# Kernel tuning notes

Hardware: AMD Instinct MI355X
Metric: run time of the kernel (lower is better)

Reference implementation:

```python
import jax, jax.numpy as jnp
import numpy as np

B, T, D, H = 2, 2048, 2048, 16


def setup_inputs() -> dict:
    key = jax.random.key(0)
    ks = jax.random.split(key, 5)
    s = 0.02  # typical init scale
    return {
        "x": jax.random.normal(ks[0], (B, T, D), jnp.float32),
        "wq": jax.random.normal(ks[1], (D, D), jnp.float32) * s,
        "wk": jax.random.normal(ks[2], (D, D), jnp.float32) * s,
        "wv": jax.random.normal(ks[3], (D, D), jnp.float32) * s,
        "wo": jax.random.normal(ks[4], (D, D), jnp.float32) * s,
    }


def weight_quant(w):
    # BitNet ternary-ish quant: sign(w) * mean(|w|), straight-through estimator
    scale = jnp.maximum(jnp.mean(jnp.abs(w)), 1e-5)
    q = jnp.sign(w) * scale
    return jax.lax.stop_gradient(q) + w - jax.lax.stop_gradient(w)


def reference(x, wq, wk, wv, wo):
    b, t, c = x.shape
    h = H
    hd = c // h
    # F.linear: y = x @ w.T  (weight shape [out, in])
    def proj(w):
        y = jnp.einsum('btc,dc->btd', x, weight_quant(w))
        return y.reshape(b, t, h, hd).transpose(0, 2, 1, 3)  # [b,h,t,hd]

    q, k, v = proj(wq), proj(wk), proj(wv)
    scale = 1.0 / np.sqrt(hd).astype(np.float32)
    scores = jnp.einsum('bhqd,bhkd->bhqk', q, k) * scale
    causal = jnp.tril(jnp.ones((t, t), dtype=bool))
    scores = jnp.where(causal, scores, jnp.finfo(scores.dtype).min)
    att = jax.nn.softmax(scores, axis=-1)
    y = jnp.einsum('bhqk,bhkd->bhqd', att, v)
    y = y.transpose(0, 2, 1, 3).reshape(b, t, c)
    return jnp.einsum('btc,dc->btd', y, weight_quant(wo))
```

## Files before the change

### kernel.cpp

```cpp
#include <hip/hip_runtime.h>
#include <stdint.h>

#define D_MODEL 2048
#define SEQ     2048
#define BATCH   2
#define NH      16
#define HD      128
#define M_TOT   (BATCH*SEQ)
#define NELEM_W (D_MODEL*D_MODEL)

typedef float f32x4 __attribute__((ext_vector_type(4)));
typedef short bf16x8 __attribute__((ext_vector_type(8)));

__device__ __forceinline__ unsigned short f2bf(float f) {
  union { float f; uint32_t u; } v; v.f = f;
  uint32_t r = v.u + 0x7FFFu + ((v.u >> 16) & 1u);
  return (unsigned short)(r >> 16);
}

__device__ __forceinline__ void gload_lds16(const unsigned short* g, unsigned short* l) {
  __builtin_amdgcn_global_load_lds(
      (const __attribute__((address_space(1))) unsigned int*)g,
      (__attribute__((address_space(3))) unsigned int*)l, 16, 0, 0);
}

__global__ __launch_bounds__(256) void reduce1(const float* w0, const float* w1,
                                               const float* w2, const float* w3,
                                               float* partials) {
  const int wi = blockIdx.y;
  const float* w = (wi == 0) ? w0 : (wi == 1) ? w1 : (wi == 2) ? w2 : w3;
  const float4* w4 = (const float4*)w;
  const int t = threadIdx.x, bx = blockIdx.x;
  float s = 0.f;
  #pragma unroll
  for (int i = 0; i < 16; ++i) {
    float4 v = w4[(size_t)bx * 4096 + i * 256 + t];
    s += fabsf(v.x) + fabsf(v.y) + fabsf(v.z) + fabsf(v.w);
  }
  #pragma unroll
  for (int off = 32; off; off >>= 1) s += __shfl_down(s, off);
  __shared__ float sm[4];
  if ((t & 63) == 0) sm[t >> 6] = s;
  __syncthreads();
  if (t == 0) partials[wi * 256 + bx] = sm[0] + sm[1] + sm[2] + sm[3];
}

__global__ __launch_bounds__(256) void reduce2(const float* partials, float* scales) {
  const int wi = blockIdx.x, t = threadIdx.x;
  float s = partials[wi * 256 + t];
  #pragma unroll
  for (int off = 32; off; off >>= 1) s += __shfl_down(s, off);
  __shared__ float sm[4];
  if ((t & 63) == 0) sm[t >> 6] = s;
  __syncthreads();
  if (t == 0) scales[wi] = fmaxf((sm[0] + sm[1] + sm[2] + sm[3]) * (1.f / 4194304.f), 1e-5f);
}

__global__ __launch_bounds__(256) void cvt_x(const float* x, unsigned short* xb) {
  const int i = blockIdx.x * 256 + threadIdx.x;
  float4 v = ((const float4*)x)[i];
  ushort4 o;
  o.x = f2bf(v.x); o.y = f2bf(v.y); o.z = f2bf(v.z); o.w = f2bf(v.w);
  ((ushort4*)xb)[i] = o;
}

__global__ __launch_bounds__(256) void sign_w(const float* w0, const float* w1,
                                              const float* w2, const float* w3,
                                              unsigned short* signs) {
  const int wi = blockIdx.y;
  const float* w = (wi == 0) ? w0 : (wi == 1) ? w1 : (wi == 2) ? w2 : w3;
  unsigned short* o = signs + (size_t)wi * NELEM_W;
  const int i = blockIdx.x * 256 + threadIdx.x;
  float4 v = ((const float4*)w)[i];
  ushort4 s;
  s.x = (v.x > 0.f) ? 0x3F80u : ((v.x < 0.f) ? 0xBF80u : 0u);
  s.y = (v.y > 0.f) ? 0x3F80u : ((v.y < 0.f) ? 0xBF80u : 0u);
  s.z = (v.z > 0.f) ? 0x3F80u : ((v.z < 0.f) ? 0xBF80u : 0u);
  s.w = (v.w > 0.f) ? 0x3F80u : ((v.w < 0.f) ? 0xBF80u : 0u);
  ((ushort4*)o)[i] = s;
}

template <int MODE>
__global__ __launch_bounds__(256) void gemm_bt(const unsigned short* __restrict__ A,
                                               const unsigned short* __restrict__ W,
                                               void* __restrict__ outp,
                                               const float* __restrict__ scales,
                                               int sidx, float extra) {
  constexpr int K = 2048;
  __shared__ alignas(16) unsigned short ldsA[128 * 64];
  __shared__ alignas(16) unsigned short ldsB[128 * 64];
  const int t = threadIdx.x;
  const int wid = t >> 6, lane = t & 63;
  const int llo = lane & 15, lhi = lane >> 4;
  const int m0 = blockIdx.y * 128, n0 = blockIdx.x * 128;
  const int wm = (wid >> 1) * 64, wn = (wid & 1) * 64;
  f32x4 acc[4][4] = {};

  for (int kt = 0; kt < K / 64; ++kt) {
    const int k0 = kt * 64;
    #pragma unroll
    for (int i = 0; i < 4; ++i) {
      const int idx = i * 256 + t;
      const int row = idx >> 3, slot = idx & 7;
      const int ksw = k0 + ((slot ^ (row & 7)) << 3);
      gload_lds16(A + (size_t)(m0 + row) * K + ksw, &ldsA[(i * 256 + wid * 64) * 8]);
      gload_lds16(W + (size_t)(n0 + row) * K + ksw, &ldsB[(i * 256 + wid * 64) * 8]);
    }
    __syncthreads();
    #pragma unroll
    for (int kk = 0; kk < 2; ++kk) {
      bf16x8 a[4], b[4];
      #pragma unroll
      for (int f = 0; f < 4; ++f) {
        const int ra = wm + f * 16 + llo;
        a[f] = *(const bf16x8*)&ldsA[ra * 64 + ((kk * 4 + lhi) ^ (ra & 7)) * 8];
        const int rb = wn + f * 16 + llo;
        b[f] = *(const bf16x8*)&ldsB[rb * 64 + ((kk * 4 + lhi) ^ (rb & 7)) * 8];
      }
      #pragma unroll
      for (int fm = 0; fm < 4; ++fm)
        #pragma unroll
        for (int fn = 0; fn < 4; ++fn)
          acc[fm][fn] = __builtin_amdgcn_mfma_f32_16x16x32_bf16(a[fm], b[fn], acc[fm][fn], 0, 0, 0);
    }
    __syncthreads();
  }

  const float sc = scales[sidx] * extra;
  #pragma unroll
  for (int fm = 0; fm < 4; ++fm)
    #pragma unroll
    for (int fn = 0; fn < 4; ++fn)
      #pragma unroll
      for (int r = 0; r < 4; ++r) {
        const int row = m0 + wm + fm * 16 + lhi * 4 + r;
        const int col = n0 + wn + fn * 16 + llo;
        const float v = acc[fm][fn][r] * sc;
        if (MODE == 2) {
          ((float*)outp)[(size_t)row * D_MODEL + col] = v;
        } else {
          const int b = row >> 11, tt = row & 2047, h = col >> 7, d = col & 127;
          size_t idx;
          if (MODE == 0) idx = ((size_t)((b * NH + h) * SEQ + tt)) * HD + d;
          else           idx = ((size_t)((b * NH + h) * HD + d)) * SEQ + tt;
          ((unsigned short*)outp)[idx] = f2bf(v);
        }
      }
}

__global__ __launch_bounds__(512, 4) void attn_fwd(const unsigned short* __restrict__ Q,
                                                   const unsigned short* __restrict__ Kt,
                                                   const unsigned short* __restrict__ VT,
                                                   unsigned short* __restrict__ O) {
  __shared__ alignas(16) unsigned short lds[2][16384];
  __shared__ alignas(16) unsigned short plds[8][1024];
  const int t = threadIdx.x;
  const int wid = t >> 6, lane = t & 63;
  const int llo = lane & 15, lhi = lane >> 4;
  const int bh = blockIdx.x;
  const int g = 15 - (int)blockIdx.y;
  const int qbase = g * 128;
  const int nt = 2 * g + 2;
  const size_t bh_td = (size_t)bh * SEQ * HD;
  const size_t bh_dt = (size_t)bh * HD * SEQ;
  unsigned short* pw = &plds[wid][0];
  const int fvl = (llo & 7) ^ ((llo & 8) >> 1);

  auto stage = [&](int buf, int j) {
    const int t0 = j * 64;
    #pragma unroll
    for (int i = 0; i < 2; ++i) {
      const int c = i * 512 + t;
      const int row = c >> 4, slot = c & 15;
      gload_lds16(Kt + bh_td + (size_t)(t0 + row) * HD + ((slot ^ (row & 15)) << 3),
                  &lds[buf][(size_t)(i * 512 + wid * 64) * 8]);
    }
    #pragma unroll
    for (int i = 0; i < 2; ++i) {
      const int c = i * 512 + t;
      const int vrow = c >> 3, vslot = c & 7;
      const int fv = (vrow & 7) ^ ((vrow & 8) >> 1);
      gload_lds16(VT + bh_dt + (size_t)vrow * SEQ + t0 + ((vslot ^ fv) << 3),
                  &lds[buf][8192 + (size_t)(i * 512 + wid * 64) * 8]);
    }
  };

  bf16x8 qa[4];
  {
    const unsigned short* qp = Q + bh_td + (size_t)(qbase + wid * 16 + llo) * HD + lhi * 8;
    #pragma unroll
    for (int kk = 0; kk < 4; ++kk) qa[kk] = *(const bf16x8*)(qp + kk * 32);
  }
  f32x4 oacc[8] = {};
  float m_r[4], l_r[4];
  #pragma unroll
  for (int r = 0; r < 4; ++r) { m_r[r] = -1e30f; l_r[r] = 0.f; }

  stage(0, 0);
  for (int j = 0; j < nt; ++j) {
    const int cur = j & 1;
    __syncthreads();
    if (j + 1 < nt) stage(cur ^ 1, j + 1);
    f32x4 s[4] = {};
    __builtin_amdgcn_s_setprio(1);
    #pragma unroll
    for (int nb = 0; nb < 4; ++nb) {
      const int row = nb * 16 + llo;
      #pragma unroll
      for (int kk = 0; kk < 4; ++kk) {
        const bf16x8 kb = *(const bf16x8*)&lds[cur][row * 128 + (((kk * 4 + lhi) ^ llo) << 3)];
        s[nb] = __builtin_amdgcn_mfma_f32_16x16x32_bf16(qa[kk], kb, s[nb], 0, 0, 0);
      }
    }
    __builtin_amdgcn_s_setprio(0);
    if (j >= nt - 2) {
      #pragma unroll
      for (int nb = 0; nb < 4; ++nb)
        #pragma unroll
        for (int r = 0; r < 4; ++r)
          if (j * 64 + nb * 16 + llo > qbase + wid * 16 + lhi * 4 + r) s[nb][r] = -1e30f;
    }
    float mx[4], al[4], ps[4];
    #pragma unroll
    for (int r = 0; r < 4; ++r)
      mx[r] = fmaxf(fmaxf(s[0][r], s[1][r]), fmaxf(s[2][r], s[3][r]));
    #pragma unroll
    for (int off = 1; off < 16; off <<= 1)
      #pragma unroll
      for (int r = 0; r < 4; ++r) mx[r] = fmaxf(mx[r], __shfl_xor(mx[r], off));
    #pragma unroll
    for (int r = 0; r < 4; ++r) {
      const float mn = fmaxf(m_r[r], mx[r]);
      al[r] = __expf(m_r[r] - mn);
      m_r[r] = mn;
      #pragma unroll
      for (int nb = 0; nb < 4; ++nb) s[nb][r] = __expf(s[nb][r] - mn);
      ps[r] = (s[0][r] + s[1][r]) + (s[2][r] + s[3][r]);
    }
    #pragma unroll
    for (int off = 1; off < 16; off <<= 1)
      #pragma unroll
      for (int r = 0; r < 4; ++r) ps[r] += __shfl_xor(ps[r], off);
    #pragma unroll
    for (int r = 0; r < 4; ++r) l_r[r] = l_r[r] * al[r] + ps[r];
    #pragma unroll
    for (int nb = 0; nb < 8; ++nb)
      #pragma unroll
      for (int r = 0; r < 4; ++r) oacc[nb][r] *= al[r];
    #pragma unroll
    for (int nb = 0; nb < 4; ++nb)
      #pragma unroll
      for (int r = 0; r < 4; ++r) {
        const int q = lhi * 4 + r;
        const int slot = nb * 2 + (llo >> 3);
        pw[q * 64 + ((slot ^ (q & 7)) << 3) + (llo & 7)] = f2bf(s[nb][r]);
      }
    asm volatile("s_waitcnt lgkmcnt(0)" ::: "memory");
    __builtin_amdgcn_sched_barrier(0);
    const bf16x8 pa0 = *(const bf16x8*)&pw[llo * 64 + ((lhi ^ (llo & 7)) << 3)];
    const bf16x8 pa1 = *(const bf16x8*)&pw[llo * 64 + (((4 + lhi) ^ (llo & 7)) << 3)];
    __builtin_amdgcn_s_setprio(1);
    #pragma unroll
    for (int db = 0; db < 8; ++db) {
      const unsigned short* vbp = &lds[cur][8192 + (db * 16 + llo) * 64];
      const bf16x8 vb0 = *(const bf16x8*)&vbp[(lhi ^ fvl) << 3];
      const bf16x8 vb1 = *(const bf16x8*)&vbp[((4 + lhi) ^ fvl) << 3];
      oacc[db] = __builtin_amdgcn_mfma_f32_16x16x32_bf16(pa0, vb0, oacc[db], 0, 0, 0);
      oacc[db] = __builtin_amdgcn_mfma_f32_16x16x32_bf16(pa1, vb1, oacc[db], 0, 0, 0);
    }
    __builtin_amdgcn_s_setprio(0);
  }

  const int b = bh >> 4, h = bh & 15;
  float inv[4];
  #pragma unroll
  for (int r = 0; r < 4; ++r) inv[r] = 1.f / l_r[r];
  #pragma unroll
  for (int db = 0; db < 8; ++db)
    #pragma unroll
    for (int r = 0; r < 4; ++r) {
      const int qi = qbase + wid * 16 + lhi * 4 + r;
      const int d = db * 16 + llo;
      O[((size_t)(b * SEQ + qi)) * D_MODEL + h * HD + d] = f2bf(oacc[db][r] * inv[r]);
    }
}

extern "C" void kernel_launch(void* const* d_in, const int* in_sizes, int n_in,
                              void* d_out, int out_size, void* d_ws, size_t ws_size,
                              hipStream_t stream) {
  const float* x  = (const float*)d_in[0];
  const float* wq = (const float*)d_in[1];
  const float* wk = (const float*)d_in[2];
  const float* wv = (const float*)d_in[3];
  const float* wo = (const float*)d_in[4];

  char* ws = (char*)d_ws;
  float* scales   = (float*)ws;
  float* partials = (float*)(ws + 256);
  unsigned short* xbf   = (unsigned short*)(ws + 8192);
  const size_t nMD = (size_t)M_TOT * D_MODEL;
  unsigned short* signs = xbf + nMD;
  unsigned short* Qb = signs + 4 * (size_t)NELEM_W;
  unsigned short* Kb = Qb + nMD;
  unsigned short* Vt = Kb + nMD;
  unsigned short* Ab = Vt + nMD;

  reduce1<<<dim3(256, 4), 256, 0, stream>>>(wq, wk, wv, wo, partials);
  reduce2<<<dim3(4), 256, 0, stream>>>(partials, scales);
  cvt_x<<<dim3(8192), 256, 0, stream>>>(x, xbf);
  sign_w<<<dim3(4096, 4), 256, 0, stream>>>(wq, wk, wv, wo, signs);

  gemm_bt<0><<<dim3(16, 32), 256, 0, stream>>>(xbf, signs,                       (void*)Qb, scales, 0, 0.08838834764831845f);
  gemm_bt<0><<<dim3(16, 32), 256, 0, stream>>>(xbf, signs + (size_t)NELEM_W,     (void*)Kb, scales, 1, 1.0f);
  gemm_bt<1><<<dim3(16, 32), 256, 0, stream>>>(xbf, signs + 2 * (size_t)NELEM_W, (void*)Vt, scales, 2, 1.0f);

  attn_fwd<<<dim3(32, 16), 512, 0, stream>>>(Qb, Kb, Vt, Ab);

  gemm_bt<2><<<dim3(16, 32), 256, 0, stream>>>(Ab, signs + 3 * (size_t)NELEM_W, d_out, scales, 3, 1.0f);
}
```

Baseline: 321.3 us.

## Fuse weight abs-sum into sign kernel and transpose attention score layout

Folds the per-weight abs-mean reduction into the sign conversion kernel, removing one full pass over the four weight matrices. The attention kernel swaps the MFMA operand order so each lane holds one query row's scores. This reduces the softmax row reductions to two cross-lane shuffles and writes P to LDS as packed 64-bit stores. It also adds a lazy rescale that only updates the running max when it grows by more than a threshold, and remaps the 1D grid of blocks. The lazy-max trick keeps exponent arguments bounded but changes numerics slightly, and partials storage grows, so the workspace offset moves.

```diff
diff --git a/kernel.cpp b/kernel.cpp
--- a/kernel.cpp
+++ b/kernel.cpp
@@ -24,53 +24,14 @@
       (__attribute__((address_space(3))) unsigned int*)l, 16, 0, 0);
 }
 
-__global__ __launch_bounds__(256) void reduce1(const float* w0, const float* w1,
-                                               const float* w2, const float* w3,
-                                               float* partials) {
-  const int wi = blockIdx.y;
-  const float* w = (wi == 0) ? w0 : (wi == 1) ? w1 : (wi == 2) ? w2 : w3;
-  const float4* w4 = (const float4*)w;
-  const int t = threadIdx.x, bx = blockIdx.x;
-  float s = 0.f;
-  #pragma unroll
-  for (int i = 0; i < 16; ++i) {
-    float4 v = w4[(size_t)bx * 4096 + i * 256 + t];
-    s += fabsf(v.x) + fabsf(v.y) + fabsf(v.z) + fabsf(v.w);
-  }
-  #pragma unroll
-  for (int off = 32; off; off >>= 1) s += __shfl_down(s, off);
-  __shared__ float sm[4];
-  if ((t & 63) == 0) sm[t >> 6] = s;
-  __syncthreads();
-  if (t == 0) partials[wi * 256 + bx] = sm[0] + sm[1] + sm[2] + sm[3];
-}
-
-__global__ __launch_bounds__(256) void reduce2(const float* partials, float* scales) {
-  const int wi = blockIdx.x, t = threadIdx.x;
-  float s = partials[wi * 256 + t];
-  #pragma unroll
-  for (int off = 32; off; off >>= 1) s += __shfl_down(s, off);
-  __shared__ float sm[4];
-  if ((t & 63) == 0) sm[t >> 6] = s;
-  __syncthreads();
-  if (t == 0) scales[wi] = fmaxf((sm[0] + sm[1] + sm[2] + sm[3]) * (1.f / 4194304.f), 1e-5f);
-}
-
-__global__ __launch_bounds__(256) void cvt_x(const float* x, unsigned short* xb) {
-  const int i = blockIdx.x * 256 + threadIdx.x;
-  float4 v = ((const float4*)x)[i];
-  ushort4 o;
-  o.x = f2bf(v.x); o.y = f2bf(v.y); o.z = f2bf(v.z); o.w = f2bf(v.w);
-  ((ushort4*)xb)[i] = o;
-}
-
 __global__ __launch_bounds__(256) void sign_w(const float* w0, const float* w1,
                                               const float* w2, const float* w3,
-                                              unsigned short* signs) {
+                                              unsigned short* signs, float* partials) {
   const int wi = blockIdx.y;
   const float* w = (wi == 0) ? w0 : (wi == 1) ? w1 : (wi == 2) ? w2 : w3;
   unsigned short* o = signs + (size_t)wi * NELEM_W;
-  const int i = blockIdx.x * 256 + threadIdx.x;
+  const int t = threadIdx.x;
+  const int i = blockIdx.x * 256 + t;
   float4 v = ((const float4*)w)[i];
   ushort4 s;
   s.x = (v.x > 0.f) ? 0x3F80u : ((v.x < 0.f) ? 0xBF80u : 0u);
@@ -78,6 +39,34 @@
   s.z = (v.z > 0.f) ? 0x3F80u : ((v.z < 0.f) ? 0xBF80u : 0u);
   s.w = (v.w > 0.f) ? 0x3F80u : ((v.w < 0.f) ? 0xBF80u : 0u);
   ((ushort4*)o)[i] = s;
+  float a = fabsf(v.x) + fabsf(v.y) + fabsf(v.z) + fabsf(v.w);
+  #pragma unroll
+  for (int off = 32; off; off >>= 1) a += __shfl_down(a, off);
+  __shared__ float sm[4];
+  if ((t & 63) == 0) sm[t >> 6] = a;
+  __syncthreads();
+  if (t == 0) partials[wi * 4096 + blockIdx.x] = sm[0] + sm[1] + sm[2] + sm[3];
+}
+
+__global__ __launch_bounds__(256) void reduce2(const float* partials, float* scales) {
+  const int wi = blockIdx.x, t = threadIdx.x;
+  float s = 0.f;
+  #pragma unroll
+  for (int i = 0; i < 16; ++i) s += partials[wi * 4096 + i * 256 + t];
+  #pragma unroll
+  for (int off = 32; off; off >>= 1) s += __shfl_down(s, off);
+  __shared__ float sm[4];
+  if ((t & 63) == 0) sm[t >> 6] = s;
+  __syncthreads();
+  if (t == 0) scales[wi] = fmaxf((sm[0] + sm[1] + sm[2] + sm[3]) * (1.f / 4194304.f), 1e-5f);
+}
+
+__global__ __launch_bounds__(256) void cvt_x(const float* x, unsigned short* xb) {
+  const int i = blockIdx.x * 256 + threadIdx.x;
+  float4 v = ((const float4*)x)[i];
+  ushort4 o;
+  o.x = f2bf(v.x); o.y = f2bf(v.y); o.z = f2bf(v.z); o.w = f2bf(v.w);
+  ((ushort4*)xb)[i] = o;
 }
 
 template <int MODE>
@@ -157,14 +146,17 @@
   const int t = threadIdx.x;
   const int wid = t >> 6, lane = t & 63;
   const int llo = lane & 15, lhi = lane >> 4;
-  const int bh = blockIdx.x;
-  const int g = 15 - (int)blockIdx.y;
+  const int j0 = blockIdx.x;
+  int bh, g;
+  if (j0 < 256) { bh = j0 & 31; g = 15 - (j0 >> 5); }
+  else          { bh = (j0 - 256) & 31; g = (j0 - 256) >> 5; }
   const int qbase = g * 128;
   const int nt = 2 * g + 2;
   const size_t bh_td = (size_t)bh * SEQ * HD;
   const size_t bh_dt = (size_t)bh * HD * SEQ;
   unsigned short* pw = &plds[wid][0];
   const int fvl = (llo & 7) ^ ((llo & 8) >> 1);
+  const int pkey = llo & 14;
 
   auto stage = [&](int buf, int j) {
     const int t0 = j * 64;
@@ -192,9 +184,7 @@
     for (int kk = 0; kk < 4; ++kk) qa[kk] = *(const bf16x8*)(qp + kk * 32);
   }
   f32x4 oacc[8] = {};
-  float m_r[4], l_r[4];
-  #pragma unroll
-  for (int r = 0; r < 4; ++r) { m_r[r] = -1e30f; l_r[r] = 0.f; }
+  float m_r = -1e30f, l_r = 0.f;
 
   stage(0, 0);
   for (int j = 0; j < nt; ++j) {
@@ -209,56 +199,56 @@
       #pragma unroll
       for (int kk = 0; kk < 4; ++kk) {
         const bf16x8 kb = *(const bf16x8*)&lds[cur][row * 128 + (((kk * 4 + lhi) ^ llo) << 3)];
-        s[nb] = __builtin_amdgcn_mfma_f32_16x16x32_bf16(qa[kk], kb, s[nb], 0, 0, 0);
+        s[nb] = __builtin_amdgcn_mfma_f32_16x16x32_bf16(kb, qa[kk], s[nb], 0, 0, 0);
       }
     }
     __builtin_amdgcn_s_setprio(0);
     if (j >= nt - 2) {
+      const int q = qbase + wid * 16 + llo;
       #pragma unroll
       for (int nb = 0; nb < 4; ++nb)
         #pragma unroll
         for (int r = 0; r < 4; ++r)
-          if (j * 64 + nb * 16 + llo > qbase + wid * 16 + lhi * 4 + r) s[nb][r] = -1e30f;
-    }
-    float mx[4], al[4], ps[4];
-    #pragma unroll
-    for (int r = 0; r < 4; ++r)
-      mx[r] = fmaxf(fmaxf(s[0][r], s[1][r]), fmaxf(s[2][r], s[3][r]));
-    #pragma unroll
-    for (int off = 1; off < 16; off <<= 1)
-      #pragma unroll
-      for (int r = 0; r < 4; ++r) mx[r] = fmaxf(mx[r], __shfl_xor(mx[r], off));
-    #pragma unroll
-    for (int r = 0; r < 4; ++r) {
-      const float mn = fmaxf(m_r[r], mx[r]);
-      al[r] = __expf(m_r[r] - mn);
-      m_r[r] = mn;
-      #pragma unroll
-      for (int nb = 0; nb < 4; ++nb) s[nb][r] = __expf(s[nb][r] - mn);
-      ps[r] = (s[0][r] + s[1][r]) + (s[2][r] + s[3][r]);
-    }
-    #pragma unroll
-    for (int off = 1; off < 16; off <<= 1)
-      #pragma unroll
-      for (int r = 0; r < 4; ++r) ps[r] += __shfl_xor(ps[r], off);
-    #pragma unroll
-    for (int r = 0; r < 4; ++r) l_r[r] = l_r[r] * al[r] + ps[r];
-    #pragma unroll
-    for (int nb = 0; nb < 8; ++nb)
-      #pragma unroll
-      for (int r = 0; r < 4; ++r) oacc[nb][r] *= al[r];
+          if (j * 64 + nb * 16 + lhi * 4 + r > q) s[nb][r] = -1e30f;
+    }
+    float mloc = -1e30f;
     #pragma unroll
     for (int nb = 0; nb < 4; ++nb)
       #pragma unroll
-      for (int r = 0; r < 4; ++r) {
-        const int q = lhi * 4 + r;
-        const int slot = nb * 2 + (llo >> 3);
-        pw[q * 64 + ((slot ^ (q & 7)) << 3) + (llo & 7)] = f2bf(s[nb][r]);
-      }
+      for (int r = 0; r < 4; ++r) mloc = fmaxf(mloc, s[nb][r]);
+    mloc = fmaxf(mloc, __shfl_xor(mloc, 16));
+    mloc = fmaxf(mloc, __shfl_xor(mloc, 32));
+    float alq = 1.f;
+    if (__any(mloc > m_r + 8.f)) {
+      const float mn = fmaxf(m_r, mloc);
+      alq = __expf(m_r - mn);
+      m_r = mn;
+      float alr[4];
+      #pragma unroll
+      for (int r = 0; r < 4; ++r) alr[r] = __shfl(alq, lhi * 4 + r);
+      #pragma unroll
+      for (int db = 0; db < 8; ++db)
+        #pragma unroll
+        for (int r = 0; r < 4; ++r) oacc[db][r] *= alr[r];
+    }
+    float ps = 0.f;
+    #pragma unroll
+    for (int nb = 0; nb < 4; ++nb) {
+      const float p0 = __expf(s[nb][0] - m_r), p1 = __expf(s[nb][1] - m_r);
+      const float p2 = __expf(s[nb][2] - m_r), p3 = __expf(s[nb][3] - m_r);
+      ps += (p0 + p1) + (p2 + p3);
+      uint2 uu;
+      uu.x = (uint32_t)f2bf(p0) | ((uint32_t)f2bf(p1) << 16);
+      uu.y = (uint32_t)f2bf(p2) | ((uint32_t)f2bf(p3) << 16);
+      *(uint2*)&pw[llo * 64 + (((nb * 4 + lhi) ^ pkey) << 2)] = uu;
+    }
+    ps += __shfl_xor(ps, 16);
+    ps += __shfl_xor(ps, 32);
+    l_r = l_r * alq + ps;
     asm volatile("s_waitcnt lgkmcnt(0)" ::: "memory");
     __builtin_amdgcn_sched_barrier(0);
-    const bf16x8 pa0 = *(const bf16x8*)&pw[llo * 64 + ((lhi ^ (llo & 7)) << 3)];
-    const bf16x8 pa1 = *(const bf16x8*)&pw[llo * 64 + (((4 + lhi) ^ (llo & 7)) << 3)];
+    const bf16x8 pa0 = *(const bf16x8*)&pw[llo * 64 + (((lhi * 2) ^ pkey) << 2)];
+    const bf16x8 pa1 = *(const bf16x8*)&pw[llo * 64 + (((8 + lhi * 2) ^ pkey) << 2)];
     __builtin_amdgcn_s_setprio(1);
     #pragma unroll
     for (int db = 0; db < 8; ++db) {
@@ -272,16 +262,17 @@
   }
 
   const int b = bh >> 4, h = bh & 15;
-  float inv[4];
-  #pragma unroll
-  for (int r = 0; r < 4; ++r) inv[r] = 1.f / l_r[r];
+  const float invq = 1.f / l_r;
+  float invr[4];
+  #pragma unroll
+  for (int r = 0; r < 4; ++r) invr[r] = __shfl(invq, lhi * 4 + r);
   #pragma unroll
   for (int db = 0; db < 8; ++db)
     #pragma unroll
     for (int r = 0; r < 4; ++r) {
       const int qi = qbase + wid * 16 + lhi * 4 + r;
       const int d = db * 16 + llo;
-      O[((size_t)(b * SEQ + qi)) * D_MODEL + h * HD + d] = f2bf(oacc[db][r] * inv[r]);
+      O[((size_t)(b * SEQ + qi)) * D_MODEL + h * HD + d] = f2bf(oacc[db][r] * invr[r]);
     }
 }
 
@@ -297,7 +288,7 @@
   char* ws = (char*)d_ws;
   float* scales   = (float*)ws;
   float* partials = (float*)(ws + 256);
-  unsigned short* xbf   = (unsigned short*)(ws + 8192);
+  unsigned short* xbf   = (unsigned short*)(ws + 131072);
   const size_t nMD = (size_t)M_TOT * D_MODEL;
   unsigned short* signs = xbf + nMD;
   unsigned short* Qb = signs + 4 * (size_t)NELEM_W;
@@ -305,16 +296,15 @@
   unsigned short* Vt = Kb + nMD;
   unsigned short* Ab = Vt + nMD;
 
-  reduce1<<<dim3(256, 4), 256, 0, stream>>>(wq, wk, wv, wo, partials);
+  sign_w<<<dim3(4096, 4), 256, 0, stream>>>(wq, wk, wv, wo, signs, partials);
   reduce2<<<dim3(4), 256, 0, stream>>>(partials, scales);
   cvt_x<<<dim3(8192), 256, 0, stream>>>(x, xbf);
-  sign_w<<<dim3(4096, 4), 256, 0, stream>>>(wq, wk, wv, wo, signs);
 
   gemm_bt<0><<<dim3(16, 32), 256, 0, stream>>>(xbf, signs,                       (void*)Qb, scales, 0, 0.08838834764831845f);
   gemm_bt<0><<<dim3(16, 32), 256, 0, stream>>>(xbf, signs + (size_t)NELEM_W,     (void*)Kb, scales, 1, 1.0f);
   gemm_bt<1><<<dim3(16, 32), 256, 0, stream>>>(xbf, signs + 2 * (size_t)NELEM_W, (void*)Vt, scales, 2, 1.0f);
 
-  attn_fwd<<<dim3(32, 16), 512, 0, stream>>>(Qb, Kb, Vt, Ab);
+  attn_fwd<<<dim3(512), 512, 0, stream>>>(Qb, Kb, Vt, Ab);
 
   gemm_bt<2><<<dim3(16, 32), 256, 0, stream>>>(Ab, signs + 3 * (size_t)NELEM_W, d_out, scales, 3, 1.0f);
 }
```

Result: faster. 261.9 us (-18.5%).
